# Optimization experiments

Measured on AMD Instinct MI355X. Metric: run time of the kernel, lower is better.

## Reference

```python
import jax, jax.numpy as jnp
import numpy as np

LEVELS = 2
BS = 8                 # block_size == plane_h == plane_w
NORMALS = (0, 1, 2)    # axis-aligned plane normals within each block
TAU = 0.05
INV_SQRT2 = 0.7071067811865476

# ---------- 1D orthonormal Haar along an axis ----------

def _dwt1(x, axis):
    x = jnp.moveaxis(x, axis, -1)
    a, b = x[..., 0::2], x[..., 1::2]
    lo = (a + b) * INV_SQRT2
    hi = (a - b) * INV_SQRT2
    return jnp.moveaxis(lo, -1, axis), jnp.moveaxis(hi, -1, axis)


def _idwt1(lo, hi, axis):
    lo = jnp.moveaxis(lo, axis, -1)
    hi = jnp.moveaxis(hi, axis, -1)
    even = (lo + hi) * INV_SQRT2
    odd = (lo - hi) * INV_SQRT2
    y = jnp.stack([even, odd], axis=-1).reshape(lo.shape[:-1] + (lo.shape[-1] * 2,))
    return jnp.moveaxis(y, -1, axis)

# ---------- one level of separable 3D Haar (8 subbands) ----------

def _dwt3_level(x):
    ld, hd = _dwt1(x, -3)
    out = {}
    for dn, db in (('l', ld), ('h', hd)):
        lh, hh = _dwt1(db, -2)
        for hn, hb in (('l', lh), ('h', hh)):
            lw, hw = _dwt1(hb, -1)
            out[dn + hn + 'l'] = lw
            out[dn + hn + 'h'] = hw
    return out


def _idwt3_level(bands):
    rec_h = {dn + hn: _idwt1(bands[dn + hn + 'l'], bands[dn + hn + 'h'], -1)
             for dn in 'lh' for hn in 'lh'}
    rec_d = {dn: _idwt1(rec_h[dn + 'l'], rec_h[dn + 'h'], -2) for dn in 'lh'}
    return _idwt1(rec_d['l'], rec_d['h'], -3)

# ---------- full multi-level 2D Haar on the last two dims (planes) ----------

def _haar2_fwd(p):
    s = p.shape[-1]
    out = p
    while s > 1:
        sub = out[..., :s, :s]
        a, b = sub[..., 0::2, :], sub[..., 1::2, :]
        sub = jnp.concatenate([(a + b) * INV_SQRT2, (a - b) * INV_SQRT2], axis=-2)
        a, b = sub[..., :, 0::2], sub[..., :, 1::2]
        sub = jnp.concatenate([(a + b) * INV_SQRT2, (a - b) * INV_SQRT2], axis=-1)
        out = out.at[..., :s, :s].set(sub)
        s //= 2
    return out


def _haar2_inv(c):
    s_full = c.shape[-1]
    out = c
    s = 2
    while s <= s_full:
        sub = out[..., :s, :s]
        lo, hi = sub[..., :, :s // 2], sub[..., :, s // 2:]
        even = (lo + hi) * INV_SQRT2
        odd = (lo - hi) * INV_SQRT2
        sub = jnp.stack([even, odd], axis=-1).reshape(sub.shape[:-1] + (s,))
        lo, hi = sub[..., :s // 2, :], sub[..., s // 2:, :]
        even = (lo + hi) * INV_SQRT2
        odd = (lo - hi) * INV_SQRT2
        sub = jnp.stack([even, odd], axis=-2).reshape(sub.shape[:-2] + (s, s))
        out = out.at[..., :s, :s].set(sub)
        s *= 2
    return out

# ---------- block extraction / assembly ----------

def _extract_blocks(band, bs):
    B, C, D, H, W = band.shape
    pd, ph, pw = (-D) % bs, (-H) % bs, (-W) % bs
    band = jnp.pad(band, ((0, 0), (0, 0), (0, pd), (0, ph), (0, pw)), mode='edge')
    nd, nh, nw = (D + pd) // bs, (H + ph) // bs, (W + pw) // bs
    blk = band.reshape(B, C, nd, bs, nh, bs, nw, bs).transpose(0, 1, 2, 4, 6, 3, 5, 7)
    return blk.reshape(-1, bs, bs, bs), (B, C, D, H, W), (nd, nh, nw)


def _assemble_blocks(blocks, orig, nblk, bs):
    B, C, D, H, W = orig
    nd, nh, nw = nblk
    x = blocks.reshape(B, C, nd, nh, nw, bs, bs, bs).transpose(0, 1, 2, 5, 3, 6, 4, 7)
    x = x.reshape(B, C, nd * bs, nh * bs, nw * bs)
    return x[:, :, :D, :H, :W]

# ---------- planewise bandlet analysis / synthesis ----------

def _analyze(blocks):
    # for each normal axis n: slice cube into planes perpendicular to n, 2D Haar each plane
    return jnp.stack([_haar2_fwd(jnp.moveaxis(blocks, 1 + n, 1)) for n in NORMALS], axis=1)


def _synthesize(packed):
    recs = [jnp.moveaxis(_haar2_inv(packed[:, i]), 1, 1 + n) for i, n in enumerate(NORMALS)]
    acc = recs[0]
    for r in recs[1:]:
        acc = acc + r
    return acc / len(NORMALS)


def _soft_threshold(c, tau):
    dc = c[..., 0, 0]  # keep per-plane DC coefficient
    t = jnp.sign(c) * jnp.maximum(jnp.abs(c) - tau, 0.0)
    return t.at[..., 0, 0].set(dc)

# ---------- full encode -> threshold -> reconstruct ----------

def _forward(x):
    B, C, D, H, W = x.shape
    mult = 2 ** LEVELS
    pd, ph, pw = (-D) % mult, (-H) % mult, (-W) % mult
    xp = jnp.pad(x, ((0, 0), (0, 0), (0, pd), (0, ph), (0, pw)), mode='reflect')
    approx = xp
    levels = []
    for _ in range(LEVELS):
        bands = _dwt3_level(approx)
        approx = bands.pop('lll')
        levels.append(bands)
    rec_levels = []
    for bands in levels:
        rec = {}
        for name, band in bands.items():
            blocks, orig, nblk = _extract_blocks(band, BS)
            packed = _soft_threshold(_analyze(blocks), TAU)
            rec[name] = _assemble_blocks(_synthesize(packed), orig, nblk, BS)
        rec_levels.append(rec)
    y = approx
    for bands in reversed(rec_levels):
        bands = dict(bands)
        bands['lll'] = y
        y = _idwt3_level(bands)
    return y[:, :, :D, :H, :W]


def setup_inputs() -> dict:
    key = jax.random.key(0)
    x = jax.random.normal(key, (2, 1, 160, 160, 160), dtype=jnp.float32)
    return {"x": x}


def reference(x):
    return _forward(x)
```

## Files before the change

### kernel.cpp

```cpp
#include <hip/hip_runtime.h>

#define IS2 0.7071067811865476f
#define C3F 0.35355339059327373f
#define TAU_F 0.05f

__device__ __forceinline__ void haar2_fwd(float (&m)[64]) {
    float t[64];
    #pragma unroll
    for (int half = 4; half >= 1; half >>= 1) {
        const int sz = half * 2;
        #pragma unroll
        for (int r = 0; r < half; ++r)
            #pragma unroll
            for (int c = 0; c < sz; ++c) {
                float a = m[(2*r)*8 + c], b = m[(2*r+1)*8 + c];
                t[r*8 + c]        = (a + b) * IS2;
                t[(r+half)*8 + c] = (a - b) * IS2;
            }
        #pragma unroll
        for (int r = 0; r < sz; ++r)
            #pragma unroll
            for (int c = 0; c < sz; ++c) m[r*8+c] = t[r*8+c];
        #pragma unroll
        for (int r = 0; r < sz; ++r)
            #pragma unroll
            for (int c = 0; c < half; ++c) {
                float a = m[r*8 + 2*c], b = m[r*8 + 2*c + 1];
                t[r*8 + c]        = (a + b) * IS2;
                t[r*8 + c + half] = (a - b) * IS2;
            }
        #pragma unroll
        for (int r = 0; r < sz; ++r)
            #pragma unroll
            for (int c = 0; c < sz; ++c) m[r*8+c] = t[r*8+c];
    }
}

__device__ __forceinline__ void haar2_inv(float (&m)[64]) {
    float t[64];
    #pragma unroll
    for (int sz = 2; sz <= 8; sz <<= 1) {
        const int half = sz >> 1;
        #pragma unroll
        for (int r = 0; r < sz; ++r)
            #pragma unroll
            for (int c = 0; c < half; ++c) {
                float lo = m[r*8 + c], hi = m[r*8 + c + half];
                t[r*8 + 2*c]     = (lo + hi) * IS2;
                t[r*8 + 2*c + 1] = (lo - hi) * IS2;
            }
        #pragma unroll
        for (int r = 0; r < sz; ++r)
            #pragma unroll
            for (int c = 0; c < sz; ++c) m[r*8+c] = t[r*8+c];
        #pragma unroll
        for (int r = 0; r < half; ++r)
            #pragma unroll
            for (int c = 0; c < sz; ++c) {
                float lo = m[r*8 + c], hi = m[(r+half)*8 + c];
                t[(2*r)*8 + c]   = (lo + hi) * IS2;
                t[(2*r+1)*8 + c] = (lo - hi) * IS2;
            }
        #pragma unroll
        for (int r = 0; r < sz; ++r)
            #pragma unroll
            for (int c = 0; c < sz; ++c) m[r*8+c] = t[r*8+c];
    }
}

__device__ __forceinline__ void bandlet_slice(float (&m)[64]) {
    haar2_fwd(m);
    float dc = m[0];
    #pragma unroll
    for (int e = 0; e < 64; ++e) {
        float v = m[e];
        float av = fabsf(v) - TAU_F;
        m[e] = av > 0.0f ? copysignf(av, v) : 0.0f;
    }
    m[0] = dc;
    haar2_inv(m);
}

__device__ __forceinline__ void bandlet_core(float* __restrict__ L, int s,
                                             bool valid, float (&a)[64]) {
    float g[64], w[64];
    if (valid) {
        #pragma unroll
        for (int r = 0; r < 8; ++r) {
            float4 v0 = *(const float4*)&L[s*64 + r*8];
            float4 v1 = *(const float4*)&L[s*64 + r*8 + 4];
            a[r*8+0]=v0.x; a[r*8+1]=v0.y; a[r*8+2]=v0.z; a[r*8+3]=v0.w;
            a[r*8+4]=v1.x; a[r*8+5]=v1.y; a[r*8+6]=v1.z; a[r*8+7]=v1.w;
        }
        bandlet_slice(a);
        #pragma unroll
        for (int r = 0; r < 8; ++r)
            #pragma unroll
            for (int c = 0; c < 8; ++c)
                g[r*8+c] = L[r*64 + c*8 + s];
        bandlet_slice(g);
        #pragma unroll
        for (int r = 0; r < 8; ++r) {
            float4 v0 = *(const float4*)&L[r*64 + s*8];
            float4 v1 = *(const float4*)&L[r*64 + s*8 + 4];
            w[r*8+0]=v0.x; w[r*8+1]=v0.y; w[r*8+2]=v0.z; w[r*8+3]=v0.w;
            w[r*8+4]=v1.x; w[r*8+5]=v1.y; w[r*8+6]=v1.z; w[r*8+7]=v1.w;
        }
    }
    __syncthreads();
    if (valid) {
        #pragma unroll
        for (int r = 0; r < 8; ++r)
            #pragma unroll
            for (int c = 0; c < 8; ++c)
                L[r*64 + c*8 + s] = g[r*8+c];
        bandlet_slice(w);
    }
    __syncthreads();
    if (valid) {
        #pragma unroll
        for (int r = 0; r < 8; ++r) {
            float4 v0 = *(const float4*)&L[s*64 + r*8];
            float4 v1 = *(const float4*)&L[s*64 + r*8 + 4];
            a[r*8+0]+=v0.x; a[r*8+1]+=v0.y; a[r*8+2]+=v0.z; a[r*8+3]+=v0.w;
            a[r*8+4]+=v1.x; a[r*8+5]+=v1.y; a[r*8+6]+=v1.z; a[r*8+7]+=v1.w;
        }
    }
    __syncthreads();
    if (valid) {
        #pragma unroll
        for (int r = 0; r < 8; ++r) {
            *(float4*)&L[r*64 + s*8]     = make_float4(w[r*8+0], w[r*8+1], w[r*8+2], w[r*8+3]);
            *(float4*)&L[r*64 + s*8 + 4] = make_float4(w[r*8+4], w[r*8+5], w[r*8+6], w[r*8+7]);
        }
    }
    __syncthreads();
    if (valid) {
        #pragma unroll
        for (int r = 0; r < 8; ++r) {
            float4 v0 = *(const float4*)&L[s*64 + r*8];
            float4 v1 = *(const float4*)&L[s*64 + r*8 + 4];
            a[r*8+0]+=v0.x; a[r*8+1]+=v0.y; a[r*8+2]+=v0.z; a[r*8+3]+=v0.w;
            a[r*8+4]+=v1.x; a[r*8+5]+=v1.y; a[r*8+6]+=v1.z; a[r*8+7]+=v1.w;
        }
    }
}

__global__ __launch_bounds__(64, 2) void fwd1_bp(const float* __restrict__ x,
                                                 float* __restrict__ bands) {
    constexpr int LST = 516;
    constexpr size_t B1S = (size_t)2 * 80 * 80 * 80;
    __shared__ __align__(16) float lin[7 * LST];

    const int t  = threadIdx.x;
    const int wg = blockIdx.x;
    const int b  = wg / 1000;
    const int tl = wg - b * 1000;
    const int td = tl / 100;
    const int rr = tl - td * 100;
    const int th = rr / 10;
    const int tw = rr - th * 10;
    const int j = t >> 3, w = t & 7;

    const float* ip = x + ((size_t)(b*160 + 16*td)) * 25600 + (size_t)(16*th) * 160 + 16*tw;
    float* lllp = bands + ((size_t)(b*80 + 8*td)) * 6400 + (size_t)(8*th) * 80 + 8*tw;

    #pragma unroll
    for (int q = 0; q < 8; ++q) {
        const float* p = ip + (size_t)(2*q) * 25600 + (2*j) * 160 + 2*w;
        float2 q00 = *(const float2*)(p);
        float2 q01 = *(const float2*)(p + 160);
        float2 q10 = *(const float2*)(p + 25600);
        float2 q11 = *(const float2*)(p + 25600 + 160);
        float wl00 = q00.x + q00.y, wh00 = q00.x - q00.y;
        float wl01 = q01.x + q01.y, wh01 = q01.x - q01.y;
        float wl10 = q10.x + q10.y, wh10 = q10.x - q10.y;
        float wl11 = q11.x + q11.y, wh11 = q11.x - q11.y;
        float hl0l = wl00 + wl01, hh0l = wl00 - wl01;
        float hl0h = wh00 + wh01, hh0h = wh00 - wh01;
        float hl1l = wl10 + wl11, hh1l = wl10 - wl11;
        float hl1h = wh10 + wh11, hh1h = wh10 - wh11;
        const int pos = q*64 + j*8 + w;
        lin[0*LST + pos] = (hl0h + hl1h) * C3F;
        lin[1*LST + pos] = (hh0l + hh1l) * C3F;
        lin[2*LST + pos] = (hh0h + hh1h) * C3F;
        lin[3*LST + pos] = (hl0l - hl1l) * C3F;
        lin[4*LST + pos] = (hl0h - hl1h) * C3F;
        lin[5*LST + pos] = (hh0l - hh1l) * C3F;
        lin[6*LST + pos] = (hh0h - hh1h) * C3F;
        lllp[q*6400 + j*80 + w] = (hl0l + hl1l) * C3F;
    }
    __syncthreads();

    const int nbp = t >> 3, s = t & 7;
    const bool valid = nbp < 7;
    float a[64];
    bandlet_core(&lin[(valid ? nbp : 0) * LST], s, valid, a);

    if (valid) {
        float* gp = bands + (size_t)(nbp + 1) * B1S
                  + ((size_t)(b*80 + 8*td + s)) * 6400 + (size_t)(8*th) * 80 + 8*tw;
        #pragma unroll
        for (int jj = 0; jj < 8; ++jj) {
            float* qo = gp + jj * 80;
            *(float4*)(qo)     = make_float4(a[jj*8+0]*(1.0f/3.0f), a[jj*8+1]*(1.0f/3.0f),
                                             a[jj*8+2]*(1.0f/3.0f), a[jj*8+3]*(1.0f/3.0f));
            *(float4*)(qo + 4) = make_float4(a[jj*8+4]*(1.0f/3.0f), a[jj*8+5]*(1.0f/3.0f),
                                             a[jj*8+6]*(1.0f/3.0f), a[jj*8+7]*(1.0f/3.0f));
        }
    }
}

__global__ __launch_bounds__(64, 2) void l2_pipeline(float* __restrict__ lll) {
    constexpr int LST = 516;
    __shared__ __align__(16) float lin[8 * LST];

    const int t  = threadIdx.x;
    const int wg = blockIdx.x;
    const int b  = wg / 125;
    const int tl = wg - b * 125;
    const int td = tl / 25;
    const int rr = tl - td * 25;
    const int th = rr / 5;
    const int tw = rr - th * 5;
    const int j = t >> 3, w = t & 7;

    float* base = lll + ((size_t)(b*80 + 16*td)) * 6400 + (size_t)(16*th) * 80 + 16*tw;

    #pragma unroll
    for (int q = 0; q < 8; ++q) {
        const float* p = base + (size_t)(2*q) * 6400 + (2*j) * 80 + 2*w;
        float2 q00 = *(const float2*)(p);
        float2 q01 = *(const float2*)(p + 80);
        float2 q10 = *(const float2*)(p + 6400);
        float2 q11 = *(const float2*)(p + 6400 + 80);
        float wl00 = q00.x + q00.y, wh00 = q00.x - q00.y;
        float wl01 = q01.x + q01.y, wh01 = q01.x - q01.y;
        float wl10 = q10.x + q10.y, wh10 = q10.x - q10.y;
        float wl11 = q11.x + q11.y, wh11 = q11.x - q11.y;
        float hl0l = wl00 + wl01, hh0l = wl00 - wl01;
        float hl0h = wh00 + wh01, hh0h = wh00 - wh01;
        float hl1l = wl10 + wl11, hh1l = wl10 - wl11;
        float hl1h = wh10 + wh11, hh1h = wh10 - wh11;
        const int pos = q*64 + j*8 + w;
        lin[0*LST + pos] = (hl0l + hl1l) * C3F;
        lin[1*LST + pos] = (hl0h + hl1h) * C3F;
        lin[2*LST + pos] = (hh0l + hh1l) * C3F;
        lin[3*LST + pos] = (hh0h + hh1h) * C3F;
        lin[4*LST + pos] = (hl0l - hl1l) * C3F;
        lin[5*LST + pos] = (hl0h - hl1h) * C3F;
        lin[6*LST + pos] = (hh0l - hh1l) * C3F;
        lin[7*LST + pos] = (hh0h - hh1h) * C3F;
    }
    __syncthreads();

    const int nbp = t >> 3, s = t & 7;
    const bool valid = nbp < 7;
    float a[64];
    bandlet_core(&lin[(valid ? nbp + 1 : 0) * LST], s, valid, a);

    __syncthreads();
    if (valid) {
        float* L = &lin[(nbp + 1) * LST];
        #pragma unroll
        for (int jj = 0; jj < 8; ++jj) {
            *(float4*)&L[s*64 + jj*8]     = make_float4(a[jj*8+0]*(1.0f/3.0f), a[jj*8+1]*(1.0f/3.0f),
                                                        a[jj*8+2]*(1.0f/3.0f), a[jj*8+3]*(1.0f/3.0f));
            *(float4*)&L[s*64 + jj*8 + 4] = make_float4(a[jj*8+4]*(1.0f/3.0f), a[jj*8+5]*(1.0f/3.0f),
                                                        a[jj*8+6]*(1.0f/3.0f), a[jj*8+7]*(1.0f/3.0f));
        }
    }
    __syncthreads();

    #pragma unroll
    for (int q = 0; q < 8; ++q) {
        const int pos = q*64 + j*8 + w;
        float b0 = lin[0*LST + pos], b1 = lin[1*LST + pos];
        float b2 = lin[2*LST + pos], b3 = lin[3*LST + pos];
        float b4 = lin[4*LST + pos], b5 = lin[5*LST + pos];
        float b6 = lin[6*LST + pos], b7 = lin[7*LST + pos];
        float c0 = b0 + b4, c1 = b1 + b5, c2 = b2 + b6, c3 = b3 + b7;
        float c4 = b0 - b4, c5 = b1 - b5, c6 = b2 - b6, c7 = b3 - b7;
        float e00 = c0 + c2, e01 = c1 + c3;
        float e02 = c0 - c2, e03 = c1 - c3;
        float e10 = c4 + c6, e11 = c5 + c7;
        float e12 = c4 - c6, e13 = c5 - c7;
        float* pp = base + (size_t)(2*q) * 6400 + (2*j) * 80 + 2*w;
        *(float2*)(pp)             = make_float2((e00+e01)*C3F, (e00-e01)*C3F);
        *(float2*)(pp + 80)        = make_float2((e02+e03)*C3F, (e02-e03)*C3F);
        *(float2*)(pp + 6400)      = make_float2((e10+e11)*C3F, (e10-e11)*C3F);
        *(float2*)(pp + 6400 + 80) = make_float2((e12+e13)*C3F, (e12-e13)*C3F);
    }
}

__global__ __launch_bounds__(256) void dwt3_inv80(const float* __restrict__ bands,
                                                  float* __restrict__ out) {
    const int tid = blockIdx.x * blockDim.x + threadIdx.x;
    constexpr int S = 80;
    const int w = tid % S;
    const int h = (tid / S) % S;
    const int d = (tid / (S*S)) % S;
    const int b = tid / (S*S*S);
    constexpr size_t bs_ = (size_t)2 * S * S * S;
    const size_t o = (size_t)tid;

    float b0 = bands[0*bs_+o], b1 = bands[1*bs_+o], b2 = bands[2*bs_+o], b3 = bands[3*bs_+o];
    float b4 = bands[4*bs_+o], b5 = bands[5*bs_+o], b6 = bands[6*bs_+o], b7 = bands[7*bs_+o];
    float c0 = b0 + b4, c1 = b1 + b5, c2 = b2 + b6, c3 = b3 + b7;
    float c4 = b0 - b4, c5 = b1 - b5, c6 = b2 - b6, c7 = b3 - b7;
    float e00 = c0 + c2, e01 = c1 + c3;
    float e02 = c0 - c2, e03 = c1 - c3;
    float e10 = c4 + c6, e11 = c5 + c7;
    float e12 = c4 - c6, e13 = c5 - c7;
    constexpr int IS = 2 * S;
    float* p = out + (((size_t)b * IS + 2*d) * IS + 2*h) * IS + 2*w;
    *(float2*)(p)                      = make_float2((e00+e01)*C3F, (e00-e01)*C3F);
    *(float2*)(p + IS)                 = make_float2((e02+e03)*C3F, (e02-e03)*C3F);
    *(float2*)(p + (size_t)IS*IS)      = make_float2((e10+e11)*C3F, (e10-e11)*C3F);
    *(float2*)(p + (size_t)IS*IS + IS) = make_float2((e12+e13)*C3F, (e12-e13)*C3F);
}

extern "C" void kernel_launch(void* const* d_in, const int* in_sizes, int n_in,
                              void* d_out, int out_size, void* d_ws, size_t ws_size,
                              hipStream_t stream) {
    const float* x = (const float*)d_in[0];
    float* out = (float*)d_out;
    float* bands = (float*)d_ws;

    fwd1_bp<<<2000, 64, 0, stream>>>(x, bands);
    l2_pipeline<<<250, 64, 0, stream>>>(bands);
    dwt3_inv80<<<4000, 256, 0, stream>>>(bands, out);
}
```

Baseline: 117.1 us.

## Restructure bandlet core into phased passes with shared accumulator, widen inverse DWT

The bandlet core now processes the three plane orientations one after another. Each orientation uses a single 64-float register array and accumulates its result into a new shared-memory buffer, where the old code held three 64-float arrays live at once. This is meant to cut register pressure and spilling, at the cost of doubling shared-memory use and adding shared read-modify-write traffic. Separately, the final inverse DWT kernel handles two coefficients per thread with float2 loads and wider stores, launching half as many threads.

```diff
diff --git a/kernel.cpp b/kernel.cpp
--- a/kernel.cpp
+++ b/kernel.cpp
@@ -81,67 +81,65 @@
     haar2_inv(m);
 }
 
-__device__ __forceinline__ void bandlet_core(float* __restrict__ L, int s,
-                                             bool valid, float (&a)[64]) {
-    float g[64], w[64];
+__device__ __forceinline__ void bandlet_phased(float* __restrict__ L,
+                                               float* __restrict__ A,
+                                               int s, bool valid,
+                                               float (&outv)[64]) {
+    {
+        float m[64];
+        if (valid) {
+            #pragma unroll
+            for (int r = 0; r < 8; ++r)
+                #pragma unroll
+                for (int c = 0; c < 8; ++c)
+                    m[r*8+c] = L[r*64 + c*8 + s];
+            bandlet_slice(m);
+            #pragma unroll
+            for (int r = 0; r < 8; ++r)
+                #pragma unroll
+                for (int c = 0; c < 8; ++c)
+                    A[r*64 + c*8 + s] = m[r*8+c];
+        }
+    }
+    __syncthreads();
+    {
+        float m[64];
+        if (valid) {
+            #pragma unroll
+            for (int r = 0; r < 8; ++r) {
+                float4 v0 = *(const float4*)&L[r*64 + s*8];
+                float4 v1 = *(const float4*)&L[r*64 + s*8 + 4];
+                m[r*8+0]=v0.x; m[r*8+1]=v0.y; m[r*8+2]=v0.z; m[r*8+3]=v0.w;
+                m[r*8+4]=v1.x; m[r*8+5]=v1.y; m[r*8+6]=v1.z; m[r*8+7]=v1.w;
+            }
+            bandlet_slice(m);
+            #pragma unroll
+            for (int r = 0; r < 8; ++r) {
+                float4 u0 = *(const float4*)&A[r*64 + s*8];
+                float4 u1 = *(const float4*)&A[r*64 + s*8 + 4];
+                u0.x+=m[r*8+0]; u0.y+=m[r*8+1]; u0.z+=m[r*8+2]; u0.w+=m[r*8+3];
+                u1.x+=m[r*8+4]; u1.y+=m[r*8+5]; u1.z+=m[r*8+6]; u1.w+=m[r*8+7];
+                *(float4*)&A[r*64 + s*8]     = u0;
+                *(float4*)&A[r*64 + s*8 + 4] = u1;
+            }
+        }
+    }
+    __syncthreads();
     if (valid) {
         #pragma unroll
         for (int r = 0; r < 8; ++r) {
             float4 v0 = *(const float4*)&L[s*64 + r*8];
             float4 v1 = *(const float4*)&L[s*64 + r*8 + 4];
-            a[r*8+0]=v0.x; a[r*8+1]=v0.y; a[r*8+2]=v0.z; a[r*8+3]=v0.w;
-            a[r*8+4]=v1.x; a[r*8+5]=v1.y; a[r*8+6]=v1.z; a[r*8+7]=v1.w;
-        }
-        bandlet_slice(a);
-        #pragma unroll
-        for (int r = 0; r < 8; ++r)
-            #pragma unroll
-            for (int c = 0; c < 8; ++c)
-                g[r*8+c] = L[r*64 + c*8 + s];
-        bandlet_slice(g);
+            outv[r*8+0]=v0.x; outv[r*8+1]=v0.y; outv[r*8+2]=v0.z; outv[r*8+3]=v0.w;
+            outv[r*8+4]=v1.x; outv[r*8+5]=v1.y; outv[r*8+6]=v1.z; outv[r*8+7]=v1.w;
+        }
+        bandlet_slice(outv);
         #pragma unroll
         for (int r = 0; r < 8; ++r) {
-            float4 v0 = *(const float4*)&L[r*64 + s*8];
-            float4 v1 = *(const float4*)&L[r*64 + s*8 + 4];
-            w[r*8+0]=v0.x; w[r*8+1]=v0.y; w[r*8+2]=v0.z; w[r*8+3]=v0.w;
-            w[r*8+4]=v1.x; w[r*8+5]=v1.y; w[r*8+6]=v1.z; w[r*8+7]=v1.w;
-        }
-    }
-    __syncthreads();
-    if (valid) {
-        #pragma unroll
-        for (int r = 0; r < 8; ++r)
-            #pragma unroll
-            for (int c = 0; c < 8; ++c)
-                L[r*64 + c*8 + s] = g[r*8+c];
-        bandlet_slice(w);
-    }
-    __syncthreads();
-    if (valid) {
-        #pragma unroll
-        for (int r = 0; r < 8; ++r) {
-            float4 v0 = *(const float4*)&L[s*64 + r*8];
-            float4 v1 = *(const float4*)&L[s*64 + r*8 + 4];
-            a[r*8+0]+=v0.x; a[r*8+1]+=v0.y; a[r*8+2]+=v0.z; a[r*8+3]+=v0.w;
-            a[r*8+4]+=v1.x; a[r*8+5]+=v1.y; a[r*8+6]+=v1.z; a[r*8+7]+=v1.w;
-        }
-    }
-    __syncthreads();
-    if (valid) {
-        #pragma unroll
-        for (int r = 0; r < 8; ++r) {
-            *(float4*)&L[r*64 + s*8]     = make_float4(w[r*8+0], w[r*8+1], w[r*8+2], w[r*8+3]);
-            *(float4*)&L[r*64 + s*8 + 4] = make_float4(w[r*8+4], w[r*8+5], w[r*8+6], w[r*8+7]);
-        }
-    }
-    __syncthreads();
-    if (valid) {
-        #pragma unroll
-        for (int r = 0; r < 8; ++r) {
-            float4 v0 = *(const float4*)&L[s*64 + r*8];
-            float4 v1 = *(const float4*)&L[s*64 + r*8 + 4];
-            a[r*8+0]+=v0.x; a[r*8+1]+=v0.y; a[r*8+2]+=v0.z; a[r*8+3]+=v0.w;
-            a[r*8+4]+=v1.x; a[r*8+5]+=v1.y; a[r*8+6]+=v1.z; a[r*8+7]+=v1.w;
+            float4 v0 = *(const float4*)&A[s*64 + r*8];
+            float4 v1 = *(const float4*)&A[s*64 + r*8 + 4];
+            outv[r*8+0]+=v0.x; outv[r*8+1]+=v0.y; outv[r*8+2]+=v0.z; outv[r*8+3]+=v0.w;
+            outv[r*8+4]+=v1.x; outv[r*8+5]+=v1.y; outv[r*8+6]+=v1.z; outv[r*8+7]+=v1.w;
         }
     }
 }
@@ -151,6 +149,7 @@
     constexpr int LST = 516;
     constexpr size_t B1S = (size_t)2 * 80 * 80 * 80;
     __shared__ __align__(16) float lin[7 * LST];
+    __shared__ __align__(16) float lacc[7 * LST];
 
     const int t  = threadIdx.x;
     const int wg = blockIdx.x;
@@ -194,8 +193,9 @@
 
     const int nbp = t >> 3, s = t & 7;
     const bool valid = nbp < 7;
-    float a[64];
-    bandlet_core(&lin[(valid ? nbp : 0) * LST], s, valid, a);
+    const int off = (valid ? nbp : 0) * LST;
+    float outv[64];
+    bandlet_phased(&lin[off], &lacc[off], s, valid, outv);
 
     if (valid) {
         float* gp = bands + (size_t)(nbp + 1) * B1S
@@ -203,10 +203,10 @@
         #pragma unroll
         for (int jj = 0; jj < 8; ++jj) {
             float* qo = gp + jj * 80;
-            *(float4*)(qo)     = make_float4(a[jj*8+0]*(1.0f/3.0f), a[jj*8+1]*(1.0f/3.0f),
-                                             a[jj*8+2]*(1.0f/3.0f), a[jj*8+3]*(1.0f/3.0f));
-            *(float4*)(qo + 4) = make_float4(a[jj*8+4]*(1.0f/3.0f), a[jj*8+5]*(1.0f/3.0f),
-                                             a[jj*8+6]*(1.0f/3.0f), a[jj*8+7]*(1.0f/3.0f));
+            *(float4*)(qo)     = make_float4(outv[jj*8+0]*(1.0f/3.0f), outv[jj*8+1]*(1.0f/3.0f),
+                                             outv[jj*8+2]*(1.0f/3.0f), outv[jj*8+3]*(1.0f/3.0f));
+            *(float4*)(qo + 4) = make_float4(outv[jj*8+4]*(1.0f/3.0f), outv[jj*8+5]*(1.0f/3.0f),
+                                             outv[jj*8+6]*(1.0f/3.0f), outv[jj*8+7]*(1.0f/3.0f));
         }
     }
 }
@@ -214,6 +214,7 @@
 __global__ __launch_bounds__(64, 2) void l2_pipeline(float* __restrict__ lll) {
     constexpr int LST = 516;
     __shared__ __align__(16) float lin[8 * LST];
+    __shared__ __align__(16) float lacc[7 * LST];
 
     const int t  = threadIdx.x;
     const int wg = blockIdx.x;
@@ -256,18 +257,19 @@
 
     const int nbp = t >> 3, s = t & 7;
     const bool valid = nbp < 7;
-    float a[64];
-    bandlet_core(&lin[(valid ? nbp + 1 : 0) * LST], s, valid, a);
+    float outv[64];
+    bandlet_phased(&lin[(valid ? nbp + 1 : 1) * LST],
+                   &lacc[(valid ? nbp : 0) * LST], s, valid, outv);
 
     __syncthreads();
     if (valid) {
         float* L = &lin[(nbp + 1) * LST];
         #pragma unroll
         for (int jj = 0; jj < 8; ++jj) {
-            *(float4*)&L[s*64 + jj*8]     = make_float4(a[jj*8+0]*(1.0f/3.0f), a[jj*8+1]*(1.0f/3.0f),
-                                                        a[jj*8+2]*(1.0f/3.0f), a[jj*8+3]*(1.0f/3.0f));
-            *(float4*)&L[s*64 + jj*8 + 4] = make_float4(a[jj*8+4]*(1.0f/3.0f), a[jj*8+5]*(1.0f/3.0f),
-                                                        a[jj*8+6]*(1.0f/3.0f), a[jj*8+7]*(1.0f/3.0f));
+            *(float4*)&L[s*64 + jj*8]     = make_float4(outv[jj*8+0]*(1.0f/3.0f), outv[jj*8+1]*(1.0f/3.0f),
+                                                        outv[jj*8+2]*(1.0f/3.0f), outv[jj*8+3]*(1.0f/3.0f));
+            *(float4*)&L[s*64 + jj*8 + 4] = make_float4(outv[jj*8+4]*(1.0f/3.0f), outv[jj*8+5]*(1.0f/3.0f),
+                                                        outv[jj*8+6]*(1.0f/3.0f), outv[jj*8+7]*(1.0f/3.0f));
         }
     }
     __syncthreads();
@@ -296,28 +298,41 @@
 __global__ __launch_bounds__(256) void dwt3_inv80(const float* __restrict__ bands,
                                                   float* __restrict__ out) {
     const int tid = blockIdx.x * blockDim.x + threadIdx.x;
-    constexpr int S = 80;
-    const int w = tid % S;
-    const int h = (tid / S) % S;
-    const int d = (tid / (S*S)) % S;
-    const int b = tid / (S*S*S);
+    constexpr int S = 80, S2 = S / 2;
+    const int w2 = tid % S2;
+    const int h  = (tid / S2) % S;
+    const int d  = (tid / (S2*S)) % S;
+    const int b  = tid / (S2*S*S);
     constexpr size_t bs_ = (size_t)2 * S * S * S;
-    const size_t o = (size_t)tid;
-
-    float b0 = bands[0*bs_+o], b1 = bands[1*bs_+o], b2 = bands[2*bs_+o], b3 = bands[3*bs_+o];
-    float b4 = bands[4*bs_+o], b5 = bands[5*bs_+o], b6 = bands[6*bs_+o], b7 = bands[7*bs_+o];
-    float c0 = b0 + b4, c1 = b1 + b5, c2 = b2 + b6, c3 = b3 + b7;
-    float c4 = b0 - b4, c5 = b1 - b5, c6 = b2 - b6, c7 = b3 - b7;
-    float e00 = c0 + c2, e01 = c1 + c3;
-    float e02 = c0 - c2, e03 = c1 - c3;
-    float e10 = c4 + c6, e11 = c5 + c7;
-    float e12 = c4 - c6, e13 = c5 - c7;
+    const size_t o = (((size_t)b * S + d) * S + h) * S + 2*w2;
+
+    float2 B0 = *(const float2*)&bands[0*bs_+o], B1 = *(const float2*)&bands[1*bs_+o];
+    float2 B2 = *(const float2*)&bands[2*bs_+o], B3 = *(const float2*)&bands[3*bs_+o];
+    float2 B4 = *(const float2*)&bands[4*bs_+o], B5 = *(const float2*)&bands[5*bs_+o];
+    float2 B6 = *(const float2*)&bands[6*bs_+o], B7 = *(const float2*)&bands[7*bs_+o];
+
     constexpr int IS = 2 * S;
-    float* p = out + (((size_t)b * IS + 2*d) * IS + 2*h) * IS + 2*w;
-    *(float2*)(p)                      = make_float2((e00+e01)*C3F, (e00-e01)*C3F);
-    *(float2*)(p + IS)                 = make_float2((e02+e03)*C3F, (e02-e03)*C3F);
-    *(float2*)(p + (size_t)IS*IS)      = make_float2((e10+e11)*C3F, (e10-e11)*C3F);
-    *(float2*)(p + (size_t)IS*IS + IS) = make_float2((e12+e13)*C3F, (e12-e13)*C3F);
+    float* p = out + (((size_t)b * IS + 2*d) * IS + 2*h) * IS + 4*w2;
+
+    #pragma unroll
+    for (int half = 0; half < 2; ++half) {
+        float b0 = half ? B0.y : B0.x, b1 = half ? B1.y : B1.x;
+        float b2 = half ? B2.y : B2.x, b3 = half ? B3.y : B3.x;
+        float b4 = half ? B4.y : B4.x, b5 = half ? B5.y : B5.x;
+        float b6 = half ? B6.y : B6.x, b7 = half ? B7.y : B7.x;
+        float c0 = b0 + b4, c1 = b1 + b5, c2 = b2 + b6, c3 = b3 + b7;
+        float c4 = b0 - b4, c5 = b1 - b5, c6 = b2 - b6, c7 = b3 - b7;
+        float e00 = c0 + c2, e01 = c1 + c3;
+        float e02 = c0 - c2, e03 = c1 - c3;
+        float e10 = c4 + c6, e11 = c5 + c7;
+        float e12 = c4 - c6, e13 = c5 - c7;
+        const int xo = 2 * half;
+        ((float2*)(p))[half]                      = make_float2((e00+e01)*C3F, (e00-e01)*C3F);
+        ((float2*)(p + IS))[half]                 = make_float2((e02+e03)*C3F, (e02-e03)*C3F);
+        ((float2*)(p + (size_t)IS*IS))[half]      = make_float2((e10+e11)*C3F, (e10-e11)*C3F);
+        ((float2*)(p + (size_t)IS*IS + IS))[half] = make_float2((e12+e13)*C3F, (e12-e13)*C3F);
+        (void)xo;
+    }
 }
 
 extern "C" void kernel_launch(void* const* d_in, const int* in_sizes, int n_in,
@@ -329,5 +344,5 @@
 
     fwd1_bp<<<2000, 64, 0, stream>>>(x, bands);
     l2_pipeline<<<250, 64, 0, stream>>>(bands);
-    dwt3_inv80<<<4000, 256, 0, stream>>>(bands, out);
-}
+    dwt3_inv80<<<2000, 256, 0, stream>>>(bands, out);
+}
```

New measurement: 125.3 us. +7.0%, slower.
